# Performance work log

Measured on AMD Instinct MI355X. Metric: run time of the kernel, lower is better.

Reference implementation:

```python
import jax, jax.numpy as jnp
import numpy as np
import math

B, N, H, D = 2, 2048, 16, 64

def setup_inputs() -> dict:
    key = jax.random.key(0)
    kq, kk, kv = jax.random.split(key, 3)
    q = jax.random.normal(kq, (B, N, H, D), dtype=jnp.float32)
    k = jax.random.normal(kk, (B, N, H, D), dtype=jnp.float32)
    v = jax.random.normal(kv, (B, N, H, D), dtype=jnp.float32)
    return {"q": q, "k": k, "v": v}

def reference(q, k, v):
    d = q.shape[-1]
    # [b,n,h,d] -> [b,h,n,d]
    qh = jnp.transpose(q, (0, 2, 1, 3))
    kh = jnp.transpose(k, (0, 2, 1, 3))
    vh = jnp.transpose(v, (0, 2, 1, 3))
    # scores: [b,h,n,n]
    scores = jnp.einsum('bhqd,bhkd->bhqk', qh, kh) / math.sqrt(d)
    # jax.nn.softmax performs the stable max-subtraction internally,
    # matching the original's explicit max-subtract + softmax.
    attn = jax.nn.softmax(scores, axis=-1)
    o = jnp.einsum('bhqk,bhkd->bhqd', attn, vh)
    # back to [b,n,h,d]
    return jnp.transpose(o, (0, 2, 1, 3))
```

## Files before the change

### kernel.cpp

```cpp
#include <hip/hip_runtime.h>


typedef float  f32x4  __attribute__((ext_vector_type(4)));
typedef float  f32x16 __attribute__((ext_vector_type(16)));
typedef short  s16x8  __attribute__((ext_vector_type(8)));
typedef short  s16x4  __attribute__((ext_vector_type(4)));
typedef int    i32x4  __attribute__((ext_vector_type(4)));

#define QSCALE 0.18033688011112042f

__device__ __forceinline__ unsigned short bf16r(float f) {
    unsigned u = __builtin_bit_cast(unsigned, f);
    u += 0x7fffu + ((u >> 16) & 1u);
    return (unsigned short)(u >> 16);
}

__device__ __forceinline__ s16x8 cvt8f(const float* p) {
    f32x4 a = *(const f32x4*)p;
    f32x4 b = *(const f32x4*)(p + 4);
    s16x8 r;
#pragma unroll
    for (int i = 0; i < 4; ++i) { r[i] = (short)bf16r(a[i]); r[i+4] = (short)bf16r(b[i]); }
    return r;
}

__device__ __forceinline__ s16x8 cvt8f_scaled(const float* p, float s) {
    f32x4 a = *(const f32x4*)p;
    f32x4 b = *(const f32x4*)(p + 4);
    s16x8 r;
#pragma unroll
    for (int i = 0; i < 4; ++i) {
        r[i]   = (short)bf16r(a[i] * s);
        r[i+4] = (short)bf16r(b[i] * s);
    }
    return r;
}

__device__ __forceinline__ void gll16(const unsigned short* g, short* l) {
    __builtin_amdgcn_global_load_lds(
        (const __attribute__((address_space(1))) unsigned int*)g,
        (__attribute__((address_space(3))) unsigned int*)l, 16, 0, 0);
}

__device__ __forceinline__ int pack2(float lo, float hi) {
    unsigned ul = __builtin_bit_cast(unsigned, lo) + 0x8000u;
    unsigned uh = __builtin_bit_cast(unsigned, hi) + 0x8000u;
    return (int)__builtin_amdgcn_perm(uh, ul, 0x07060302u);
}

__global__ void __launch_bounds__(256)
prep(const float* __restrict__ K, const float* __restrict__ V,
     unsigned short* __restrict__ Kt, unsigned short* __restrict__ Vt) {
    const int t = threadIdx.x, bid = blockIdx.x;
    const int bh = bid & 31, nb = bid >> 5;
    const int b = bh >> 4, h = bh & 15;
    const size_t tile0 = ((size_t)bh * 64 + nb * 2) * 2048;

#pragma unroll
    for (int i = 0; i < 2; ++i) {
        const int lin = t * 2 + i;
        const int kbl = lin >> 8, rem = lin & 255;
        const int r = rem >> 3, s = rem & 7;
        const int c = (s - r) & 7;
        const float* src = K + ((size_t)(b * 2048 + nb * 64 + kbl * 32 + r)) * 1024
                             + h * 64 + c * 8;
        *(s16x8*)(Kt + tile0 + kbl * 2048 + r * 64 + s * 8) = cvt8f(src);
    }

    __shared__ short tile[64 * 72];
    {
        const int l16 = t & 15, r = t >> 4;
#pragma unroll
        for (int p = 0; p < 4; ++p) {
            const int key = p * 16 + r;
            const float* vp = V + ((size_t)(b * 2048 + nb * 64 + key)) * 1024
                                + h * 64 + l16 * 4;
            f32x4 x = *(const f32x4*)vp;
#pragma unroll
            for (int i = 0; i < 4; ++i)
                tile[(l16 * 4 + i) * 72 + key] = (short)bf16r(x[i]);
        }
    }
    __syncthreads();
#pragma unroll
    for (int i = 0; i < 4; ++i) {
        const int lin = t * 4 + i;
        const int kbl = lin >> 9, rem = lin & 511;
        const int d = rem >> 3, p = rem & 7;
        const int u = (p - (d >> 1)) & 7;
        s16x4 x = *(const s16x4*)&tile[d * 72 + kbl * 32 + u * 4];
        *(s16x4*)(Vt + tile0 + kbl * 2048 + d * 32 + p * 4) = x;
    }
}

__global__ void __launch_bounds__(256, 2)
attn_fwd(const float* __restrict__ Q, const unsigned short* __restrict__ Kt,
         const unsigned short* __restrict__ Vt, float* __restrict__ O)
{
    __shared__ __align__(16) char smem[65536];

    const int t = threadIdx.x;
    const int w = t >> 6, lane = t & 63;
    const int g = lane >> 5, nl = lane & 31;
    const int qsel = w & 1, ksel = w >> 1;

    const int bid = blockIdx.x;
    const int bh  = bid & 31, qb = bid >> 5;
    const int b   = bh >> 4,  h  = bh & 15;
    const int q0  = qb * 128 + qsel * 64;

    char* wbase = smem + w * 16384;
    short* sKb[2] = { (short*)wbase,            (short*)(wbase + 4096) };
    short* sVb[2] = { (short*)(wbase + 8192),   (short*)(wbase + 12288) };

    s16x8 qf[2][4];
#pragma unroll
    for (int qt = 0; qt < 2; ++qt) {
        const float* qp = Q + ((size_t)(b * 2048 + q0 + qt * 32 + nl)) * 1024
                            + h * 64 + g * 8;
#pragma unroll
        for (int kc = 0; kc < 4; ++kc)
            qf[qt][kc] = cvt8f_scaled(qp + kc * 16, QSCALE);
    }

    int koffr[4];
#pragma unroll
    for (int kc = 0; kc < 4; ++kc)
        koffr[kc] = nl * 64 + ((2 * kc + g + nl) & 7) * 8;
    int voffr[2][2];
#pragma unroll
    for (int s = 0; s < 2; ++s) {
        voffr[s][0] = nl * 32 + (((2 * s + g)     + (nl >> 1)) & 7) * 4;
        voffr[s][1] = nl * 32 + (((4 + 2 * s + g) + (nl >> 1)) & 7) * 4;
    }

    const int lane8 = lane * 8;
    const unsigned short* gbase = Kt + (size_t)bh * 131072;
    const unsigned short* vbase = Vt + (size_t)bh * 131072;

    auto issue = [&](int it, int buf) {
        const int kb = ksel * 32 + it;
        const unsigned short* gk = gbase + (size_t)kb * 2048 + lane8;
        const unsigned short* gv = vbase + (size_t)kb * 2048 + lane8;
#pragma unroll
        for (int i = 0; i < 4; ++i) {
            gll16(gk + i * 512, sKb[buf] + i * 512);
            gll16(gv + i * 512, sVb[buf] + i * 512);
        }
    };

    issue(0, 0);

    f32x16 oa[2][2] = {};
    f32x4 lpv[2] = {};

#pragma unroll 2
    for (int it = 0; it < 32; ++it) {
        const int cur = it & 1;
        const short* bK = sKb[cur];
        const short* bV = sVb[cur];

        asm volatile("s_waitcnt vmcnt(0)" ::: "memory");

        s16x8 kf[4];
#pragma unroll
        for (int kc = 0; kc < 4; ++kc) kf[kc] = *(const s16x8*)&bK[koffr[kc]];
        s16x4 vfl[2][2], vfh[2][2];
#pragma unroll
        for (int dt = 0; dt < 2; ++dt)
#pragma unroll
            for (int s = 0; s < 2; ++s) {
                vfl[dt][s] = *(const s16x4*)&bV[dt * 1024 + voffr[s][0]];
                vfh[dt][s] = *(const s16x4*)&bV[dt * 1024 + voffr[s][1]];
            }

        if (it + 1 < 32) issue(it + 1, cur ^ 1);

        int pk[2][8];
#pragma unroll
        for (int qt = 0; qt < 2; ++qt) {
            f32x16 sacc = {};
#pragma unroll
            for (int kc = 0; kc < 4; ++kc)
                sacc = __builtin_amdgcn_mfma_f32_32x32x16_bf16(kf[kc], qf[qt][kc], sacc, 0, 0, 0);
            float p[16];
#pragma unroll
            for (int r = 0; r < 16; ++r) p[r] = __builtin_amdgcn_exp2f(sacc[r]);
#pragma unroll
            for (int i = 0; i < 4; ++i)
                lpv[qt] += (f32x4){p[4*i], p[4*i+1], p[4*i+2], p[4*i+3]};
#pragma unroll
            for (int i = 0; i < 8; ++i) pk[qt][i] = pack2(p[2*i], p[2*i+1]);
        }

#pragma unroll
        for (int dt = 0; dt < 2; ++dt)
#pragma unroll
            for (int s = 0; s < 2; ++s) {
                s16x8 a = __builtin_shufflevector(vfl[dt][s], vfh[dt][s],
                                                  0, 1, 2, 3, 4, 5, 6, 7);
#pragma unroll
                for (int qt = 0; qt < 2; ++qt) {
                    i32x4 bd = { pk[qt][s*2], pk[qt][s*2+1],
                                 pk[qt][s*2+4], pk[qt][s*2+5] };
                    oa[dt][qt] = __builtin_amdgcn_mfma_f32_32x32x16_bf16(
                        a, __builtin_bit_cast(s16x8, bd), oa[dt][qt], 0, 0, 0);
                }
            }
    }

    float lp[2] = { lpv[0][0] + lpv[0][1] + lpv[0][2] + lpv[0][3],
                    lpv[1][0] + lpv[1][1] + lpv[1][2] + lpv[1][3] };

    __syncthreads();
    float* ex = (float*)smem;
    float* zone = ex + qsel * (64 * 68) + lane * 68;
    if (ksel) {
#pragma unroll
        for (int dt = 0; dt < 2; ++dt)
#pragma unroll
            for (int qt = 0; qt < 2; ++qt)
#pragma unroll
                for (int i = 0; i < 4; ++i)
                    *(f32x4*)(zone + (dt * 2 + qt) * 16 + i * 4) =
                        (f32x4){ oa[dt][qt][4*i],   oa[dt][qt][4*i+1],
                                 oa[dt][qt][4*i+2], oa[dt][qt][4*i+3] };
        zone[64] = lp[0];
        zone[65] = lp[1];
    }
    __syncthreads();
    if (!ksel) {
#pragma unroll
        for (int dt = 0; dt < 2; ++dt)
#pragma unroll
            for (int qt = 0; qt < 2; ++qt)
#pragma unroll
                for (int i = 0; i < 4; ++i) {
                    f32x4 u = *(const f32x4*)(zone + (dt * 2 + qt) * 16 + i * 4);
#pragma unroll
                    for (int j = 0; j < 4; ++j) oa[dt][qt][4*i+j] += u[j];
                }
        float inv[2];
#pragma unroll
        for (int qt = 0; qt < 2; ++qt) {
            float s = lp[qt] + zone[64 + qt];
            s += __shfl_xor(s, 32);
            inv[qt] = 1.0f / s;
        }
#pragma unroll
        for (int qt = 0; qt < 2; ++qt) {
            float* op = O + ((size_t)(b * 2048 + q0 + qt * 32 + nl)) * 1024 + h * 64;
#pragma unroll
            for (int dt = 0; dt < 2; ++dt)
#pragma unroll
                for (int rq = 0; rq < 4; ++rq) {
                    const int d = dt * 32 + 8 * rq + 4 * g;
                    *(f32x4*)(op + d) = (f32x4){
                        oa[dt][qt][4*rq]   * inv[qt], oa[dt][qt][4*rq+1] * inv[qt],
                        oa[dt][qt][4*rq+2] * inv[qt], oa[dt][qt][4*rq+3] * inv[qt] };
                }
        }
    }
}

extern "C" void kernel_launch(void* const* d_in, const int* in_sizes, int n_in,
                              void* d_out, int out_size, void* d_ws, size_t ws_size,
                              hipStream_t stream) {
    const float* q = (const float*)d_in[0];
    const float* k = (const float*)d_in[1];
    const float* v = (const float*)d_in[2];
    float* o = (float*)d_out;

    unsigned short* Kt = (unsigned short*)d_ws;
    unsigned short* Vt = Kt + 4194304;

    hipLaunchKernelGGL(prep,     dim3(1024), dim3(256), 0, stream, k, v, Kt, Vt);
    hipLaunchKernelGGL(attn_fwd, dim3(512),  dim3(256), 0, stream, q, Kt, Vt, o);
}
```

Baseline: 134.0 us.

## Split key range across eight waves sharing K/V tiles with four-way reduction

The attention kernel grows from 256 to 512 threads. Waves now form pairs: within each pair, one wave loads the K tile and the other loads the V tile into a shared buffer, replacing the old scheme where every wave loaded its own K and V. The key range is split four ways instead of two, with a sequential three-step LDS reduction at the end. The prep kernel writes V in a new swizzled layout so each wave can fetch V fragments with single 16-byte LDS reads. pack2 uses the hardware bf16 pack instruction when the compiler provides it. The aim is more waves in flight and less duplicated global/LDS traffic, at the cost of a block-wide barrier every iteration and a longer serialized reduction.

```diff
diff --git a/kernel.cpp b/kernel.cpp
--- a/kernel.cpp
+++ b/kernel.cpp
@@ -43,9 +43,13 @@
 }
 
 __device__ __forceinline__ int pack2(float lo, float hi) {
+#if __has_builtin(__builtin_amdgcn_cvt_pk_bf16_f32)
+    return __builtin_bit_cast(int, __builtin_amdgcn_cvt_pk_bf16_f32(lo, hi));
+#else
     unsigned ul = __builtin_bit_cast(unsigned, lo) + 0x8000u;
     unsigned uh = __builtin_bit_cast(unsigned, hi) + 0x8000u;
     return (int)__builtin_amdgcn_perm(uh, ul, 0x07060302u);
+#endif
 }
 
 __global__ void __launch_bounds__(256)
@@ -83,17 +87,19 @@
     }
     __syncthreads();
 #pragma unroll
-    for (int i = 0; i < 4; ++i) {
-        const int lin = t * 4 + i;
-        const int kbl = lin >> 9, rem = lin & 511;
-        const int d = rem >> 3, p = rem & 7;
-        const int u = (p - (d >> 1)) & 7;
-        s16x4 x = *(const s16x4*)&tile[d * 72 + kbl * 32 + u * 4];
-        *(s16x4*)(Vt + tile0 + kbl * 2048 + d * 32 + p * 4) = x;
-    }
-}
-
-__global__ void __launch_bounds__(256, 2)
+    for (int i = 0; i < 2; ++i) {
+        const int lin = t * 2 + i;
+        const int kbl = lin >> 8, rem = lin & 255;
+        const int d = rem >> 2, q = rem & 3;
+        const int e = (q - d) & 3;
+        s16x4 lo = *(const s16x4*)&tile[d * 72 + kbl * 32 + 4 * e];
+        s16x4 hi = *(const s16x4*)&tile[d * 72 + kbl * 32 + 16 + 4 * e];
+        s16x8 x = __builtin_shufflevector(lo, hi, 0, 1, 2, 3, 4, 5, 6, 7);
+        *(s16x8*)(Vt + tile0 + kbl * 2048 + d * 32 + q * 8) = x;
+    }
+}
+
+__global__ void __launch_bounds__(512, 4)
 attn_fwd(const float* __restrict__ Q, const unsigned short* __restrict__ Kt,
          const unsigned short* __restrict__ Vt, float* __restrict__ O)
 {
@@ -102,16 +108,16 @@
     const int t = threadIdx.x;
     const int w = t >> 6, lane = t & 63;
     const int g = lane >> 5, nl = lane & 31;
-    const int qsel = w & 1, ksel = w >> 1;
+    const int qsel = w & 1, kq = w >> 1;
 
     const int bid = blockIdx.x;
     const int bh  = bid & 31, qb = bid >> 5;
     const int b   = bh >> 4,  h  = bh & 15;
     const int q0  = qb * 128 + qsel * 64;
 
-    char* wbase = smem + w * 16384;
-    short* sKb[2] = { (short*)wbase,            (short*)(wbase + 4096) };
-    short* sVb[2] = { (short*)(wbase + 8192),   (short*)(wbase + 12288) };
+    char* setb = smem + kq * 16384;
+    short* sKbuf[2] = { (short*)setb,            (short*)(setb + 4096) };
+    short* sVbuf[2] = { (short*)(setb + 8192),   (short*)(setb + 12288) };
 
     s16x8 qf[2][4];
 #pragma unroll
@@ -129,24 +135,20 @@
         koffr[kc] = nl * 64 + ((2 * kc + g + nl) & 7) * 8;
     int voffr[2][2];
 #pragma unroll
-    for (int s = 0; s < 2; ++s) {
-        voffr[s][0] = nl * 32 + (((2 * s + g)     + (nl >> 1)) & 7) * 4;
-        voffr[s][1] = nl * 32 + (((4 + 2 * s + g) + (nl >> 1)) & 7) * 4;
-    }
-
-    const int lane8 = lane * 8;
-    const unsigned short* gbase = Kt + (size_t)bh * 131072;
-    const unsigned short* vbase = Vt + (size_t)bh * 131072;
-
-    auto issue = [&](int it, int buf) {
-        const int kb = ksel * 32 + it;
-        const unsigned short* gk = gbase + (size_t)kb * 2048 + lane8;
-        const unsigned short* gv = vbase + (size_t)kb * 2048 + lane8;
-#pragma unroll
-        for (int i = 0; i < 4; ++i) {
-            gll16(gk + i * 512, sKb[buf] + i * 512);
-            gll16(gv + i * 512, sVb[buf] + i * 512);
-        }
+    for (int dt = 0; dt < 2; ++dt)
+#pragma unroll
+        for (int s = 0; s < 2; ++s)
+            voffr[dt][s] = (dt * 32 + nl) * 32 + (((2 * s + g) + nl) & 3) * 8;
+
+    const unsigned short* tbase = (qsel == 0 ? Kt : Vt);
+    const unsigned short* gsrc0 = tbase + ((size_t)bh * 64 + kq * 16) * 2048 + lane * 8;
+
+    auto issue = [&](int j, int buf) {
+        const unsigned short* gsrc = gsrc0 + (size_t)j * 2048;
+        short* dst = (qsel == 0 ? sKbuf[buf] : sVbuf[buf]);
+#pragma unroll
+        for (int i = 0; i < 4; ++i)
+            gll16(gsrc + i * 512, dst + i * 512);
     };
 
     issue(0, 0);
@@ -154,27 +156,23 @@
     f32x16 oa[2][2] = {};
     f32x4 lpv[2] = {};
 
-#pragma unroll 2
-    for (int it = 0; it < 32; ++it) {
-        const int cur = it & 1;
-        const short* bK = sKb[cur];
-        const short* bV = sVb[cur];
-
-        asm volatile("s_waitcnt vmcnt(0)" ::: "memory");
-
+    for (int j = 0; j < 16; ++j) {
+        const int cur = j & 1;
+        __syncthreads();
+
+        const short* bK = sKbuf[cur];
+        const short* bV = sVbuf[cur];
         s16x8 kf[4];
 #pragma unroll
         for (int kc = 0; kc < 4; ++kc) kf[kc] = *(const s16x8*)&bK[koffr[kc]];
-        s16x4 vfl[2][2], vfh[2][2];
+        s16x8 vf[2][2];
 #pragma unroll
         for (int dt = 0; dt < 2; ++dt)
 #pragma unroll
-            for (int s = 0; s < 2; ++s) {
-                vfl[dt][s] = *(const s16x4*)&bV[dt * 1024 + voffr[s][0]];
-                vfh[dt][s] = *(const s16x4*)&bV[dt * 1024 + voffr[s][1]];
-            }
-
-        if (it + 1 < 32) issue(it + 1, cur ^ 1);
+            for (int s = 0; s < 2; ++s)
+                vf[dt][s] = *(const s16x8*)&bV[voffr[dt][s]];
+
+        if (j + 1 < 16) issue(j + 1, cur ^ 1);
 
         int pk[2][8];
 #pragma unroll
@@ -197,14 +195,12 @@
         for (int dt = 0; dt < 2; ++dt)
 #pragma unroll
             for (int s = 0; s < 2; ++s) {
-                s16x8 a = __builtin_shufflevector(vfl[dt][s], vfh[dt][s],
-                                                  0, 1, 2, 3, 4, 5, 6, 7);
 #pragma unroll
                 for (int qt = 0; qt < 2; ++qt) {
                     i32x4 bd = { pk[qt][s*2], pk[qt][s*2+1],
                                  pk[qt][s*2+4], pk[qt][s*2+5] };
                     oa[dt][qt] = __builtin_amdgcn_mfma_f32_32x32x16_bf16(
-                        a, __builtin_bit_cast(s16x8, bd), oa[dt][qt], 0, 0, 0);
+                        vf[dt][s], __builtin_bit_cast(s16x8, bd), oa[dt][qt], 0, 0, 0);
                 }
             }
     }
@@ -213,37 +209,45 @@
                     lpv[1][0] + lpv[1][1] + lpv[1][2] + lpv[1][3] };
 
     __syncthreads();
-    float* ex = (float*)smem;
-    float* zone = ex + qsel * (64 * 68) + lane * 68;
-    if (ksel) {
-#pragma unroll
-        for (int dt = 0; dt < 2; ++dt)
-#pragma unroll
-            for (int qt = 0; qt < 2; ++qt)
-#pragma unroll
-                for (int i = 0; i < 4; ++i)
-                    *(f32x4*)(zone + (dt * 2 + qt) * 16 + i * 4) =
-                        (f32x4){ oa[dt][qt][4*i],   oa[dt][qt][4*i+1],
-                                 oa[dt][qt][4*i+2], oa[dt][qt][4*i+3] };
-        zone[64] = lp[0];
-        zone[65] = lp[1];
-    }
-    __syncthreads();
-    if (!ksel) {
-#pragma unroll
-        for (int dt = 0; dt < 2; ++dt)
-#pragma unroll
-            for (int qt = 0; qt < 2; ++qt)
-#pragma unroll
-                for (int i = 0; i < 4; ++i) {
-                    f32x4 u = *(const f32x4*)(zone + (dt * 2 + qt) * 16 + i * 4);
-#pragma unroll
-                    for (int j = 0; j < 4; ++j) oa[dt][qt][4*i+j] += u[j];
-                }
+    float* zone = (float*)smem + qsel * 4352 + lane * 68;
+#pragma unroll
+    for (int src = 1; src < 4; ++src) {
+        if (kq == src) {
+#pragma unroll
+            for (int dt = 0; dt < 2; ++dt)
+#pragma unroll
+                for (int qt = 0; qt < 2; ++qt)
+#pragma unroll
+                    for (int i = 0; i < 4; ++i)
+                        *(f32x4*)(zone + (dt * 2 + qt) * 16 + i * 4) =
+                            (f32x4){ oa[dt][qt][4*i],   oa[dt][qt][4*i+1],
+                                     oa[dt][qt][4*i+2], oa[dt][qt][4*i+3] };
+            zone[64] = lp[0];
+            zone[65] = lp[1];
+        }
+        __syncthreads();
+        if (kq == 0) {
+#pragma unroll
+            for (int dt = 0; dt < 2; ++dt)
+#pragma unroll
+                for (int qt = 0; qt < 2; ++qt)
+#pragma unroll
+                    for (int i = 0; i < 4; ++i) {
+                        f32x4 u = *(const f32x4*)(zone + (dt * 2 + qt) * 16 + i * 4);
+#pragma unroll
+                        for (int jj = 0; jj < 4; ++jj) oa[dt][qt][4*i+jj] += u[jj];
+                    }
+            lp[0] += zone[64];
+            lp[1] += zone[65];
+        }
+        __syncthreads();
+    }
+
+    if (kq == 0) {
         float inv[2];
 #pragma unroll
         for (int qt = 0; qt < 2; ++qt) {
-            float s = lp[qt] + zone[64 + qt];
+            float s = lp[qt];
             s += __shfl_xor(s, 32);
             inv[qt] = 1.0f / s;
         }
@@ -275,5 +279,5 @@
     unsigned short* Vt = Kt + 4194304;
 
     hipLaunchKernelGGL(prep,     dim3(1024), dim3(256), 0, stream, k, v, Kt, Vt);
-    hipLaunchKernelGGL(attn_fwd, dim3(512),  dim3(256), 0, stream, q, Kt, Vt, o);
-}
+    hipLaunchKernelGGL(attn_fwd, dim3(512),  dim3(512), 0, stream, q, Kt, Vt, o);
+}
```

Result: slower. 234.1 us (+74.7%).
